# Performance work log

Hardware: AMD Instinct MI355X
Metric: run time of the kernel (lower is better)

## Reference

```python
import jax, jax.numpy as jnp
import numpy as np

PARENTS = [-1, 0, 0, 0, 1, 2, 3, 4, 5, 6, 7, 8, 9, 9, 9, 12, 13, 14, 16, 17, 18, 19, 20, 21]
J = len(PARENTS)  # 24
B = 524288
EPS = 1e-8


def _bfs_order(parents):
    children = {i: [] for i in range(len(parents))}
    for j, p in enumerate(parents):
        if p >= 0:
            children[p].append(j)
    order = [0]
    i = 0
    while i < len(order):
        order.extend(children[order[i]])
        i += 1
    return order

BFS_ORDER = _bfs_order(PARENTS)


def setup_inputs() -> dict:
    key = jax.random.key(0)
    k1, k2, k3, k4, k5 = jax.random.split(key, 5)
    root_orientation_quat = jax.random.normal(k1, (B, 4), dtype=jnp.float32)
    root_position = jax.random.normal(k2, (B, 3), dtype=jnp.float32)
    local_joint_rotations_quat = jax.random.normal(k3, (B, J, 4), dtype=jnp.float32)
    bone_lengths = jax.random.uniform(k4, (B, J), dtype=jnp.float32, minval=0.05, maxval=0.5)
    rest_directions = jax.random.normal(k5, (J, 3), dtype=jnp.float32)
    rest_directions = rest_directions / (jnp.linalg.norm(rest_directions, axis=-1, keepdims=True) + EPS)
    return {
        'root_orientation_quat': root_orientation_quat,
        'root_position': root_position,
        'local_joint_rotations_quat': local_joint_rotations_quat,
        'bone_lengths': bone_lengths,
        'rest_directions': rest_directions,
    }


def _quat_mul(p, c):
    # Hamilton product, (w, x, y, z) layout; p, c: [B, 4]
    pw, px, py, pz = p[:, 0], p[:, 1], p[:, 2], p[:, 3]
    cw, cx, cy, cz = c[:, 0], c[:, 1], c[:, 2], c[:, 3]
    return jnp.stack([
        pw * cw - px * cx - py * cy - pz * cz,
        pw * cx + px * cw + py * cz - pz * cy,
        pw * cy - px * cz + py * cw + pz * cx,
        pw * cz + px * cy - py * cx + pz * cw,
    ], axis=-1)


def reference(root_orientation_quat, root_position, local_joint_rotations_quat, bone_lengths, rest_directions):
    root_q = root_orientation_quat / (jnp.linalg.norm(root_orientation_quat, axis=-1, keepdims=True) + EPS)
    local_q = local_joint_rotations_quat / (jnp.linalg.norm(local_joint_rotations_quat, axis=-1, keepdims=True) + EPS)

    glob_q = [None] * J
    glob_p = [None] * J
    glob_q[0] = root_q
    glob_p[0] = root_position

    for j in BFS_ORDER:
        p = PARENTS[j]
        if p == -1:
            continue
        pq = glob_q[p]              # [B, 4] parent global orientation
        glob_q[j] = _quat_mul(pq, local_q[:, j, :])
        # rotate unit rest direction by parent global quaternion:
        # v' = v + qw * t + qvec x t, where t = 2 * (qvec x v)
        qvec = pq[:, 1:]            # [B, 3]
        qw = pq[:, 0:1]             # [B, 1]
        d = rest_directions[j][None, :]  # [1, 3] broadcast over batch
        t = 2.0 * jnp.cross(qvec, jnp.broadcast_to(d, qvec.shape), axis=1)
        rotated = d + qw * t + jnp.cross(qvec, t, axis=1)
        glob_p[j] = glob_p[p] + rotated * bone_lengths[:, j:j + 1]

    return jnp.stack(glob_p, axis=1)  # [B, J, 3]
```

## Files before the change

### kernel.cpp

```cpp
#include <hip/hip_runtime.h>
#include <math.h>


#define NB 524288
#define NJ 24
#define BLOCK 128
#define STRIDE 129

namespace {
constexpr int PAR[NJ] = {-1,0,0,0,1,2,3,4,5,6,7,8,9,9,9,12,13,14,16,17,18,19,20,21};
}

__global__ __launch_bounds__(BLOCK)
void ForwardKinematics_51342039056994_kernel(
    const float* __restrict__ root_q,
    const float* __restrict__ root_p,
    const float* __restrict__ loc_q,
    const float* __restrict__ bones,
    const float* __restrict__ rest_d,
    float* __restrict__ out)
{
    __shared__ float lds[96 * STRIDE];
    __shared__ float rd[NJ * 3];

    const int tid = threadIdx.x;
    const int blockBase = blockIdx.x * BLOCK;
    const int b = blockBase + tid;

    if (tid < NJ * 3) rd[tid] = rest_d[tid];

    {
        const float4* src = (const float4*)(loc_q + (size_t)blockBase * 96);
        #pragma unroll
        for (int m = 0; m < 24; ++m) {
            int g = m * BLOCK + tid;
            float4 v = src[g];
            int t = g / 24;
            int k = 4 * (g % 24);
            lds[(k + 0) * STRIDE + t] = v.x;
            lds[(k + 1) * STRIDE + t] = v.y;
            lds[(k + 2) * STRIDE + t] = v.z;
            lds[(k + 3) * STRIDE + t] = v.w;
        }
    }

    float bl[NJ];
    {
        const float4* bsrc = (const float4*)(bones + (size_t)b * NJ);
        #pragma unroll
        for (int m = 0; m < 6; ++m) {
            float4 v = bsrc[m];
            bl[4*m+0] = v.x; bl[4*m+1] = v.y; bl[4*m+2] = v.z; bl[4*m+3] = v.w;
        }
    }

    float4 rq = ((const float4*)root_q)[b];
    float rpx = root_p[b*3+0], rpy = root_p[b*3+1], rpz = root_p[b*3+2];

    __syncthreads();

    float gqw[NJ], gqx[NJ], gqy[NJ], gqz[NJ];
    float gpx[NJ], gpy[NJ], gpz[NJ];

    {
        float inv = 1.0f / (sqrtf(rq.x*rq.x + rq.y*rq.y + rq.z*rq.z + rq.w*rq.w) + 1e-8f);
        gqw[0] = rq.x * inv; gqx[0] = rq.y * inv; gqy[0] = rq.z * inv; gqz[0] = rq.w * inv;
        gpx[0] = rpx; gpy[0] = rpy; gpz[0] = rpz;
        lds[0 * STRIDE + tid] = rpx;
        lds[1 * STRIDE + tid] = rpy;
        lds[2 * STRIDE + tid] = rpz;
    }

    #pragma unroll
    for (int j = 1; j < NJ; ++j) {
        const int p = PAR[j];
        float lw = lds[(4*j + 0) * STRIDE + tid];
        float lx = lds[(4*j + 1) * STRIDE + tid];
        float ly = lds[(4*j + 2) * STRIDE + tid];
        float lz = lds[(4*j + 3) * STRIDE + tid];
        float invn = 1.0f / (sqrtf(lw*lw + lx*lx + ly*ly + lz*lz) + 1e-8f);
        lw *= invn; lx *= invn; ly *= invn; lz *= invn;

        float pw = gqw[p], pqx = gqx[p], pqy = gqy[p], pqz = gqz[p];

        gqw[j] = pw*lw - pqx*lx - pqy*ly - pqz*lz;
        gqx[j] = pw*lx + pqx*lw + pqy*lz - pqz*ly;
        gqy[j] = pw*ly - pqx*lz + pqy*lw + pqz*lx;
        gqz[j] = pw*lz + pqx*ly - pqy*lx + pqz*lw;

        float dx = rd[3*j+0], dy = rd[3*j+1], dz = rd[3*j+2];
        float tx = 2.0f * (pqy*dz - pqz*dy);
        float ty = 2.0f * (pqz*dx - pqx*dz);
        float tz = 2.0f * (pqx*dy - pqy*dx);
        float rx = dx + pw*tx + (pqy*tz - pqz*ty);
        float ry = dy + pw*ty + (pqz*tx - pqx*tz);
        float rz = dz + pw*tz + (pqx*ty - pqy*tx);

        float L = bl[j];
        gpx[j] = gpx[p] + rx * L;
        gpy[j] = gpy[p] + ry * L;
        gpz[j] = gpz[p] + rz * L;

        lds[(4*j + 0) * STRIDE + tid] = gpx[j];
        lds[(4*j + 1) * STRIDE + tid] = gpy[j];
        lds[(4*j + 2) * STRIDE + tid] = gpz[j];
    }

    __syncthreads();

    {
        float4* dst = (float4*)(out + (size_t)blockBase * 72);
        #pragma unroll
        for (int m = 0; m < 18; ++m) {
            int g = m * BLOCK + tid;
            int t = g / 18;
            int r = 4 * (g % 18);
            float4 v;
            { int rr = r + 0; v.x = lds[(4*(rr/3) + (rr%3)) * STRIDE + t]; }
            { int rr = r + 1; v.y = lds[(4*(rr/3) + (rr%3)) * STRIDE + t]; }
            { int rr = r + 2; v.z = lds[(4*(rr/3) + (rr%3)) * STRIDE + t]; }
            { int rr = r + 3; v.w = lds[(4*(rr/3) + (rr%3)) * STRIDE + t]; }
            dst[g] = v;
        }
    }
}

extern "C" void kernel_launch(void* const* d_in, const int* in_sizes, int n_in,
                              void* d_out, int out_size, void* d_ws, size_t ws_size,
                              hipStream_t stream) {
    const float* root_q = (const float*)d_in[0];
    const float* root_p = (const float*)d_in[1];
    const float* loc_q  = (const float*)d_in[2];
    const float* bones  = (const float*)d_in[3];
    const float* rest_d = (const float*)d_in[4];
    float* out = (float*)d_out;

    dim3 grid(NB / BLOCK);
    dim3 block(BLOCK);
    ForwardKinematics_51342039056994_kernel<<<grid, block, 0, stream>>>(
        root_q, root_p, loc_q, bones, rest_d, out);
}
```

Baseline: 367.8 us.

## Drop LDS staging; load quaternions and store positions directly per thread

Removes the shared-memory transpose used to coalesce quaternion loads and position stores. Each thread now reads its own 384-byte quaternion row with float4 loads and writes its output row as float4 stores inside the joint loop, so stores interleave with compute. Block size doubles to 256 and rest directions come from global memory. This drops the LDS traffic and barriers, but per-thread strided global accesses are less coalesced within a wavefront and lean on cache to merge lines.

```diff
diff --git a/kernel.cpp b/kernel.cpp
--- a/kernel.cpp
+++ b/kernel.cpp
@@ -4,8 +4,7 @@
 
 #define NB 524288
 #define NJ 24
-#define BLOCK 128
-#define STRIDE 129
+#define BLOCK 256
 
 namespace {
 constexpr int PAR[NJ] = {-1,0,0,0,1,2,3,4,5,6,7,8,9,9,9,12,13,14,16,17,18,19,20,21};
@@ -20,64 +19,37 @@
     const float* __restrict__ rest_d,
     float* __restrict__ out)
 {
-    __shared__ float lds[96 * STRIDE];
-    __shared__ float rd[NJ * 3];
+    const int b = blockIdx.x * BLOCK + threadIdx.x;
 
-    const int tid = threadIdx.x;
-    const int blockBase = blockIdx.x * BLOCK;
-    const int b = blockBase + tid;
-
-    if (tid < NJ * 3) rd[tid] = rest_d[tid];
-
-    {
-        const float4* src = (const float4*)(loc_q + (size_t)blockBase * 96);
-        #pragma unroll
-        for (int m = 0; m < 24; ++m) {
-            int g = m * BLOCK + tid;
-            float4 v = src[g];
-            int t = g / 24;
-            int k = 4 * (g % 24);
-            lds[(k + 0) * STRIDE + t] = v.x;
-            lds[(k + 1) * STRIDE + t] = v.y;
-            lds[(k + 2) * STRIDE + t] = v.z;
-            lds[(k + 3) * STRIDE + t] = v.w;
-        }
-    }
-
-    float bl[NJ];
-    {
-        const float4* bsrc = (const float4*)(bones + (size_t)b * NJ);
-        #pragma unroll
-        for (int m = 0; m < 6; ++m) {
-            float4 v = bsrc[m];
-            bl[4*m+0] = v.x; bl[4*m+1] = v.y; bl[4*m+2] = v.z; bl[4*m+3] = v.w;
-        }
-    }
-
-    float4 rq = ((const float4*)root_q)[b];
-    float rpx = root_p[b*3+0], rpy = root_p[b*3+1], rpz = root_p[b*3+2];
-
-    __syncthreads();
+    const float4* lq   = (const float4*)loc_q + (size_t)b * NJ;
+    const float4* bsrc = (const float4*)bones + (size_t)b * (NJ/4);
+    float4*       dst  = (float4*)out + (size_t)b * 18;
 
     float gqw[NJ], gqx[NJ], gqy[NJ], gqz[NJ];
     float gpx[NJ], gpy[NJ], gpz[NJ];
 
+    float bl[NJ];
+    #pragma unroll
+    for (int m = 0; m < NJ/4; ++m) {
+        float4 v = bsrc[m];
+        bl[4*m+0] = v.x; bl[4*m+1] = v.y; bl[4*m+2] = v.z; bl[4*m+3] = v.w;
+    }
+
     {
+        float4 rq = ((const float4*)root_q)[b];
         float inv = 1.0f / (sqrtf(rq.x*rq.x + rq.y*rq.y + rq.z*rq.z + rq.w*rq.w) + 1e-8f);
         gqw[0] = rq.x * inv; gqx[0] = rq.y * inv; gqy[0] = rq.z * inv; gqz[0] = rq.w * inv;
-        gpx[0] = rpx; gpy[0] = rpy; gpz[0] = rpz;
-        lds[0 * STRIDE + tid] = rpx;
-        lds[1 * STRIDE + tid] = rpy;
-        lds[2 * STRIDE + tid] = rpz;
+        gpx[0] = root_p[b*3+0];
+        gpy[0] = root_p[b*3+1];
+        gpz[0] = root_p[b*3+2];
     }
 
     #pragma unroll
     for (int j = 1; j < NJ; ++j) {
         const int p = PAR[j];
-        float lw = lds[(4*j + 0) * STRIDE + tid];
-        float lx = lds[(4*j + 1) * STRIDE + tid];
-        float ly = lds[(4*j + 2) * STRIDE + tid];
-        float lz = lds[(4*j + 3) * STRIDE + tid];
+
+        float4 l = lq[j];
+        float lw = l.x, lx = l.y, ly = l.z, lz = l.w;
         float invn = 1.0f / (sqrtf(lw*lw + lx*lx + ly*ly + lz*lz) + 1e-8f);
         lw *= invn; lx *= invn; ly *= invn; lz *= invn;
 
@@ -88,7 +60,7 @@
         gqy[j] = pw*ly - pqx*lz + pqy*lw + pqz*lx;
         gqz[j] = pw*lz + pqx*ly - pqy*lx + pqz*lw;
 
-        float dx = rd[3*j+0], dy = rd[3*j+1], dz = rd[3*j+2];
+        float dx = rest_d[3*j+0], dy = rest_d[3*j+1], dz = rest_d[3*j+2];
         float tx = 2.0f * (pqy*dz - pqz*dy);
         float ty = 2.0f * (pqz*dx - pqx*dz);
         float tz = 2.0f * (pqx*dy - pqy*dx);
@@ -101,26 +73,11 @@
         gpy[j] = gpy[p] + ry * L;
         gpz[j] = gpz[p] + rz * L;
 
-        lds[(4*j + 0) * STRIDE + tid] = gpx[j];
-        lds[(4*j + 1) * STRIDE + tid] = gpy[j];
-        lds[(4*j + 2) * STRIDE + tid] = gpz[j];
-    }
-
-    __syncthreads();
-
-    {
-        float4* dst = (float4*)(out + (size_t)blockBase * 72);
-        #pragma unroll
-        for (int m = 0; m < 18; ++m) {
-            int g = m * BLOCK + tid;
-            int t = g / 18;
-            int r = 4 * (g % 18);
-            float4 v;
-            { int rr = r + 0; v.x = lds[(4*(rr/3) + (rr%3)) * STRIDE + t]; }
-            { int rr = r + 1; v.y = lds[(4*(rr/3) + (rr%3)) * STRIDE + t]; }
-            { int rr = r + 2; v.z = lds[(4*(rr/3) + (rr%3)) * STRIDE + t]; }
-            { int rr = r + 3; v.w = lds[(4*(rr/3) + (rr%3)) * STRIDE + t]; }
-            dst[g] = v;
+        if ((j & 3) == 3) {
+            const int g = j >> 2;
+            dst[3*g+0] = make_float4(gpx[j-3], gpy[j-3], gpz[j-3], gpx[j-2]);
+            dst[3*g+1] = make_float4(gpy[j-2], gpz[j-2], gpx[j-1], gpy[j-1]);
+            dst[3*g+2] = make_float4(gpz[j-1], gpx[j],   gpy[j],   gpz[j]);
         }
     }
 }
```

After: 482.4 us. +31.2%, slower.
